# Kernel optimization log

Hardware: AMD Instinct MI355X
Metric: run time of the kernel (lower is better)

The kernel has to match this reference:

```python
import jax, jax.numpy as jnp
import numpy as np

N = 10000      # nodes of this type
T = 160000     # total metapath instances (ragged rows)
D = 256        # input_dim
P = 256        # pre_embed_dim
H = 512        # mlp_settings['layer_list'][0]
S = 64         # select_dim


def setup_inputs() -> dict:
    key = jax.random.key(0)
    ks = jax.random.split(key, 16)
    def w(k, shape):
        return jax.random.normal(k, shape, jnp.float32) / np.sqrt(shape[0]).astype(np.float32)
    return {
        "feat_A": jax.random.normal(ks[0], (N, D), jnp.float32),
        "feat_AP": jax.random.normal(ks[1], (T, D), jnp.float32),
        "feat_APA": jax.random.normal(ks[2], (T, 2 * D), jnp.float32),
        "seg_AP": jnp.sort(jax.random.randint(ks[3], (T,), 0, N, jnp.int32)),
        "seg_APA": jnp.sort(jax.random.randint(ks[4], (T,), 0, N, jnp.int32)),
        "type_weight": w(ks[5], (D, P)),
        "W_enc_AP": w(ks[6], (D, H)),   "b_enc_AP": jnp.zeros((H,), jnp.float32),
        "W_dec_AP": w(ks[7], (H, P)),   "b_dec_AP": jnp.zeros((P,), jnp.float32),
        "W_enc_APA": w(ks[8], (2 * D, H)), "b_enc_APA": jnp.zeros((H,), jnp.float32),
        "W_dec_APA": w(ks[9], (H, P)),  "b_dec_APA": jnp.zeros((P,), jnp.float32),
        "W_attn1": w(ks[10], (2 * P, 2 * P)),
        "W_attn2": w(ks[11], (2 * P, 1)),
        "W_cls": w(ks[12], (P, S)), "b_cls": jnp.zeros((S,), jnp.float32),
    }


def reference(feat_A, feat_AP, feat_APA, seg_AP, seg_APA, type_weight,
              W_enc_AP, b_enc_AP, W_dec_AP, b_dec_AP,
              W_enc_APA, b_enc_APA, W_dec_APA, b_dec_APA,
              W_attn1, W_attn2, W_cls, b_cls):
    # center node embedding (metapath of length 1): feat @ type_weight
    center = feat_A @ type_weight                                  # [N, P]

    def metapath_path(feat, seg, We, be, Wd, bd):
        # per-metapath MLP encode (Linear+ReLU) / decode (Linear)
        h = jax.nn.relu(feat @ We + be)                            # [T, H]
        dec = h @ Wd + bd                                          # [T, P]
        # ragged split + per-node sum aggregation; empty segments -> zeros
        return jax.ops.segment_sum(dec, seg, num_segments=N,
                                   indices_are_sorted=True)        # [N, P]

    inj_AP = metapath_path(feat_AP, seg_AP, W_enc_AP, b_enc_AP, W_dec_AP, b_dec_AP)
    inj_APA = metapath_path(feat_APA, seg_APA, W_enc_APA, b_enc_APA, W_dec_APA, b_dec_APA)

    def attn_score(inj):
        # attn = Tanh -> Linear(2P,2P,no bias) -> Linear(2P,1,no bias) -> LeakyReLU(0.1), then mean
        x = jnp.tanh(jnp.concatenate([center, inj], axis=1))       # [N, 2P]
        s = (x @ W_attn1) @ W_attn2                                # [N, 1]
        return jax.nn.leaky_relu(s, 0.1).mean()

    # index 0 corresponds to the length-1 metapath (never scored; fixed to 0)
    scores = jnp.stack([jnp.zeros((), jnp.float32), attn_score(inj_AP), attn_score(inj_APA)])
    wts = jax.nn.softmax(scores)                                   # [3]

    inj_AP = inj_AP * wts[1]
    inj_APA = inj_APA * wts[2]
    embed = (inj_AP + inj_APA) * 0.5                               # stack(...,dim=2).mean(dim=2)
    pre_embed = jax.nn.log_softmax((center + embed) @ W_cls + b_cls, axis=1)  # [N, S]
    return pre_embed, inj_AP, inj_APA
```

## Files before the change

### kernel.cpp

```cpp
#include <hip/hip_runtime.h>
#include <stdint.h>

typedef __bf16 bf16x8 __attribute__((ext_vector_type(8)));
typedef __bf16 bf16x4 __attribute__((ext_vector_type(4)));
typedef float  f32x4  __attribute__((ext_vector_type(4)));

#define N_NODES 10000
#define T_ROWS  160000
#define HDIM    512
#define PDIM    256
#define NCTILES 157

__device__ __forceinline__ f32x4 mfma16(bf16x8 a, bf16x8 b, f32x4 c) {
    return __builtin_amdgcn_mfma_f32_16x16x32_bf16(a, b, c, 0, 0, 0);
}

__device__ __forceinline__ void pack_one(const float* __restrict__ W,
                                         __bf16* __restrict__ out,
                                         int K, int Nc, int ltid) {
    int lane = ltid & 63;
    int t = ltid >> 6;
    int KT = K >> 5;
    int kt = t % KT, nt = t / KT;
    int col = (nt << 4) + (lane & 15);
    int krow = (kt << 5) + ((lane >> 4) << 3);
    __bf16* dst = out + ((size_t)ltid << 3);
#pragma unroll
    for (int e = 0; e < 8; ++e)
        dst[e] = (__bf16)W[(size_t)(krow + e) * Nc + col];
}

__global__ void pack6_kernel(
    const float* __restrict__ tw,    __bf16* __restrict__ twP,
    const float* __restrict__ WeAP,  __bf16* __restrict__ WeAPp,
    const float* __restrict__ WdAP,  __bf16* __restrict__ WdAPp,
    const float* __restrict__ WeAPA, __bf16* __restrict__ WeAPAp,
    const float* __restrict__ WdAPA, __bf16* __restrict__ WdAPAp,
    const float* __restrict__ W1, const float* __restrict__ W2,
    float* __restrict__ vbuf)
{
    int tid = blockIdx.x * 512 + threadIdx.x;
    if      (tid <  8192) pack_one(tw,    twP,    256, 256, tid);
    else if (tid < 24576) pack_one(WeAP,  WeAPp,  256, 512, tid - 8192);
    else if (tid < 40960) pack_one(WdAP,  WdAPp,  512, 256, tid - 24576);
    else if (tid < 73728) pack_one(WeAPA, WeAPAp, 512, 512, tid - 40960);
    else if (tid < 90112) pack_one(WdAPA, WdAPAp, 512, 256, tid - 73728);
    else if (tid < 90624) {
        int k = tid - 90112;
        float s = 0.f;
        for (int j = 0; j < 512; ++j) s += W1[k * 512 + j] * W2[j];
        vbuf[k] = s;
    }
}

template<int DIN>
__device__ __forceinline__ void path_body(
    const float* __restrict__ X,
    const __bf16* __restrict__ WeP, const float* __restrict__ be,
    const __bf16* __restrict__ WdP, const float* __restrict__ bd,
    const int* __restrict__ seg,
    float* __restrict__ inj,
    int tile, __bf16* buf, int* segs)
{
    constexpr int LDX = DIN + 8;
    constexpr int LDH = HDIM + 8;
    constexpr int LDP = 260;
    constexpr int KT1 = DIN / 32;
    const int tid = threadIdx.x;
    const int row0 = tile * 64;
    if (tid < 64) segs[tid] = seg[row0 + tid];

#pragma unroll 4
    for (int i = tid; i < 64 * (DIN / 4); i += 512) {
        int r = i / (DIN / 4), c4 = i % (DIN / 4);
        float4 f = ((const float4*)X)[(size_t)(row0 + r) * (DIN / 4) + c4];
        bf16x4 h;
        h[0] = (__bf16)f.x; h[1] = (__bf16)f.y; h[2] = (__bf16)f.z; h[3] = (__bf16)f.w;
        *(bf16x4*)&buf[r * LDX + c4 * 4] = h;
    }
    __syncthreads();

    const int wave = tid >> 6, lane = tid & 63;
    const int lr = lane & 15, lg = lane >> 4;

    f32x4 acc1[4][4] = {};
    {
        const __bf16* w1 = WeP + ((size_t)(wave * 4) * KT1) * 512 + lane * 8;
        bf16x8 bX[4], bY[4], a[4];
#pragma unroll
        for (int ct = 0; ct < 4; ++ct) bX[ct] = *(const bf16x8*)&w1[(size_t)(ct * KT1) * 512];
        for (int kt = 0; kt < KT1; kt += 2) {
#pragma unroll
            for (int ct = 0; ct < 4; ++ct)
                bY[ct] = *(const bf16x8*)&w1[(size_t)(ct * KT1 + kt + 1) * 512];
            int ko = kt * 32 + lg * 8;
#pragma unroll
            for (int rt = 0; rt < 4; ++rt)
                a[rt] = *(const bf16x8*)&buf[(rt * 16 + lr) * LDX + ko];
            __builtin_amdgcn_s_setprio(1);
#pragma unroll
            for (int ct = 0; ct < 4; ++ct)
#pragma unroll
                for (int rt = 0; rt < 4; ++rt)
                    acc1[rt][ct] = mfma16(a[rt], bX[ct], acc1[rt][ct]);
            __builtin_amdgcn_s_setprio(0);
            int kn = (kt + 2 < KT1) ? kt + 2 : 0;
#pragma unroll
            for (int ct = 0; ct < 4; ++ct)
                bX[ct] = *(const bf16x8*)&w1[(size_t)(ct * KT1 + kn) * 512];
            ko = (kt + 1) * 32 + lg * 8;
#pragma unroll
            for (int rt = 0; rt < 4; ++rt)
                a[rt] = *(const bf16x8*)&buf[(rt * 16 + lr) * LDX + ko];
            __builtin_amdgcn_s_setprio(1);
#pragma unroll
            for (int ct = 0; ct < 4; ++ct)
#pragma unroll
                for (int rt = 0; rt < 4; ++rt)
                    acc1[rt][ct] = mfma16(a[rt], bY[ct], acc1[rt][ct]);
            __builtin_amdgcn_s_setprio(0);
        }
    }
    __syncthreads();

#pragma unroll
    for (int ct = 0; ct < 4; ++ct) {
        int col = wave * 64 + ct * 16 + lr;
        float bias = be[col];
#pragma unroll
        for (int rt = 0; rt < 4; ++rt) {
            int rbase = rt * 16 + lg * 4;
#pragma unroll
            for (int j = 0; j < 4; ++j) {
                float vl = acc1[rt][ct][j] + bias;
                buf[(rbase + j) * LDH + col] = (__bf16)(vl > 0.f ? vl : 0.f);
            }
        }
    }
    __syncthreads();

    f32x4 acc2[4][2] = {};
    {
        const __bf16* w2 = WdP + ((size_t)(wave * 2) * 16) * 512 + lane * 8;
        bf16x8 bX2[2], bY2[2], aX[4], aY[4];
#pragma unroll
        for (int ct = 0; ct < 2; ++ct) bX2[ct] = *(const bf16x8*)&w2[(size_t)(ct * 16) * 512];
#pragma unroll
        for (int rt = 0; rt < 4; ++rt)
            aX[rt] = *(const bf16x8*)&buf[(rt * 16 + lr) * LDH + lg * 8];
        for (int kt = 0; kt < 16; kt += 2) {
#pragma unroll
            for (int ct = 0; ct < 2; ++ct)
                bY2[ct] = *(const bf16x8*)&w2[(size_t)(ct * 16 + kt + 1) * 512];
            int ko = (kt + 1) * 32 + lg * 8;
#pragma unroll
            for (int rt = 0; rt < 4; ++rt)
                aY[rt] = *(const bf16x8*)&buf[(rt * 16 + lr) * LDH + ko];
            __builtin_amdgcn_s_setprio(1);
#pragma unroll
            for (int ct = 0; ct < 2; ++ct)
#pragma unroll
                for (int rt = 0; rt < 4; ++rt)
                    acc2[rt][ct] = mfma16(aX[rt], bX2[ct], acc2[rt][ct]);
            __builtin_amdgcn_s_setprio(0);
            int kn = (kt + 2 < 16) ? kt + 2 : 0;
#pragma unroll
            for (int ct = 0; ct < 2; ++ct)
                bX2[ct] = *(const bf16x8*)&w2[(size_t)(ct * 16 + kn) * 512];
            ko = kn * 32 + lg * 8;
#pragma unroll
            for (int rt = 0; rt < 4; ++rt)
                aX[rt] = *(const bf16x8*)&buf[(rt * 16 + lr) * LDH + ko];
            __builtin_amdgcn_s_setprio(1);
#pragma unroll
            for (int ct = 0; ct < 2; ++ct)
#pragma unroll
                for (int rt = 0; rt < 4; ++rt)
                    acc2[rt][ct] = mfma16(aY[rt], bY2[ct], acc2[rt][ct]);
            __builtin_amdgcn_s_setprio(0);
        }
    }
    __syncthreads();

    float* decs = (float*)buf;
#pragma unroll
    for (int ct = 0; ct < 2; ++ct) {
        int col = wave * 32 + ct * 16 + lr;
        float bias = bd[col];
#pragma unroll
        for (int rt = 0; rt < 4; ++rt) {
            int rbase = rt * 16 + lg * 4;
#pragma unroll
            for (int j = 0; j < 4; ++j)
                decs[(rbase + j) * LDP + col] = acc2[rt][ct][j] + bias;
        }
    }

    {
        const int c  = wave * 32 + (lane & 31);
        const int rs = (lane >> 5) * 32;
        float run = decs[rs * LDP + c];
        int cur = segs[rs];
        int runstart = rs;
#pragma unroll
        for (int r = rs + 1; r < rs + 32; ++r) {
            int s = segs[r];
            float v = decs[r * LDP + c];
            if (s == cur) run += v;
            else {
                if (runstart != rs) inj[(size_t)cur * PDIM + c] = run;
                else atomicAdd(&inj[(size_t)cur * PDIM + c], run);
                cur = s; run = v; runstart = r;
            }
        }
        atomicAdd(&inj[(size_t)cur * PDIM + c], run);
    }
}

__device__ __forceinline__ void center_body(
    const float* __restrict__ feat, const __bf16* __restrict__ twP,
    float* __restrict__ center, int tile, __bf16* xs)
{
    constexpr int LDX = 264;
    const int tid = threadIdx.x;
    const int row0 = tile * 64;
#pragma unroll 4
    for (int i = tid; i < 64 * 64; i += 512) {
        int r = i / 64, c4 = i % 64;
        int row = row0 + r;
        float4 f = {0.f, 0.f, 0.f, 0.f};
        if (row < N_NODES) f = ((const float4*)feat)[(size_t)row * 64 + c4];
        bf16x4 h;
        h[0] = (__bf16)f.x; h[1] = (__bf16)f.y; h[2] = (__bf16)f.z; h[3] = (__bf16)f.w;
        *(bf16x4*)&xs[r * LDX + c4 * 4] = h;
    }
    __syncthreads();

    const int wave = tid >> 6, lane = tid & 63;
    const int lr = lane & 15, lg = lane >> 4;
    f32x4 acc[4][2] = {};
    const __bf16* w = twP + ((size_t)(wave * 2) * 8) * 512 + lane * 8;
    for (int kt = 0; kt < 8; ++kt) {
        int ko = kt * 32 + lg * 8;
        bf16x8 a[4];
#pragma unroll
        for (int rt = 0; rt < 4; ++rt)
            a[rt] = *(const bf16x8*)&xs[(rt * 16 + lr) * LDX + ko];
#pragma unroll
        for (int ct = 0; ct < 2; ++ct) {
            bf16x8 b = *(const bf16x8*)&w[(size_t)(ct * 8 + kt) * 512];
#pragma unroll
            for (int rt = 0; rt < 4; ++rt)
                acc[rt][ct] = mfma16(a[rt], b, acc[rt][ct]);
        }
    }
#pragma unroll
    for (int ct = 0; ct < 2; ++ct) {
        int col = wave * 32 + ct * 16 + lr;
#pragma unroll
        for (int rt = 0; rt < 4; ++rt) {
            int rbase = rt * 16 + lg * 4;
#pragma unroll
            for (int j = 0; j < 4; ++j) {
                int row = row0 + rbase + j;
                if (row < N_NODES) center[(size_t)row * 256 + col] = acc[rt][ct][j];
            }
        }
    }
}

__global__ __launch_bounds__(512, 4) void paths_kernel(
    const float* __restrict__ featAP,  const float* __restrict__ featAPA,
    const __bf16* __restrict__ WeAPp,  const float* __restrict__ beAP,
    const __bf16* __restrict__ WdAPp,  const float* __restrict__ bdAP,
    const __bf16* __restrict__ WeAPAp, const float* __restrict__ beAPA,
    const __bf16* __restrict__ WdAPAp, const float* __restrict__ bdAPA,
    const int* __restrict__ segAP, const int* __restrict__ segAPA,
    float* __restrict__ injAP, float* __restrict__ injAPA,
    const float* __restrict__ featA, const __bf16* __restrict__ twP,
    float* __restrict__ center)
{
    __shared__ __bf16 buf[64 * (HDIM + 8)];
    __shared__ int segs[64];
    int bid = blockIdx.x;
    if (bid < NCTILES) {
        center_body(featA, twP, center, bid, buf);
        return;
    }
    int p = bid - NCTILES;
    int tile = p >> 1;
    if (p & 1)
        path_body<512>(featAPA, WeAPAp, beAPA, WdAPAp, bdAPA, segAPA, injAPA,
                       tile, buf, segs);
    else
        path_body<256>(featAP, WeAPp, beAP, WdAPp, bdAP, segAP, injAP,
                       tile, buf, segs);
}

__global__ __launch_bounds__(256, 4) void score2_kernel(
    const float* __restrict__ center, const float* __restrict__ injAP,
    const float* __restrict__ injAPA, const float* __restrict__ v,
    float* __restrict__ sacc)
{
    const int w = threadIdx.x >> 6, lane = threadIdx.x & 63;
    float l1 = 0.f, l2 = 0.f;
    for (int row = blockIdx.x * 4 + w; row < N_NODES; row += gridDim.x * 4) {
        float x1 = 0.f, x2 = 0.f;
#pragma unroll
        for (int k = 0; k < 4; ++k) {
            int c = lane + k * 64;
            size_t off = (size_t)row * 256 + c;
            float tc = tanhf(center[off]) * v[c];
            float vi = v[256 + c];
            x1 += tc + tanhf(injAP[off]) * vi;
            x2 += tc + tanhf(injAPA[off]) * vi;
        }
#pragma unroll
        for (int o = 32; o > 0; o >>= 1) {
            x1 += __shfl_xor(x1, o);
            x2 += __shfl_xor(x2, o);
        }
        if (lane == 0) {
            l1 += (x1 > 0.f) ? x1 : 0.1f * x1;
            l2 += (x2 > 0.f) ? x2 : 0.1f * x2;
        }
    }
    if (lane == 0) {
        atomicAdd(&sacc[0], l1);
        atomicAdd(&sacc[1], l2);
    }
}

__global__ __launch_bounds__(256, 4) void final_kernel(
    const float* __restrict__ center, const float* __restrict__ injAP,
    const float* __restrict__ injAPA, const float* __restrict__ sacc,
    const float* __restrict__ Wcls, const float* __restrict__ bcls,
    float* __restrict__ out0, float* __restrict__ out1, float* __restrict__ out2)
{
    __shared__ float zs[4][256];
    float s1 = sacc[0] * (1.f / N_NODES), s2 = sacc[1] * (1.f / N_NODES);
    float m0 = fmaxf(0.f, fmaxf(s1, s2));
    float e0 = expf(0.f - m0), e1 = expf(s1 - m0), e2 = expf(s2 - m0);
    float inv = 1.f / (e0 + e1 + e2);
    const float w1 = e1 * inv, w2 = e2 * inv;

    const int row0 = blockIdx.x * 4;
    for (int idx = threadIdx.x; idx < 1024; idx += 256) {
        int r = idx >> 8, c = idx & 255;
        size_t off = (size_t)(row0 + r) * 256 + c;
        float a = injAP[off] * w1, b = injAPA[off] * w2;
        out1[off] = a; out2[off] = b;
        zs[r][c] = center[off] + 0.5f * (a + b);
    }
    __syncthreads();
    const int g = threadIdx.x >> 6, j = threadIdx.x & 63;
    float logit = bcls[j];
    for (int k = 0; k < 256; ++k) logit += zs[g][k] * Wcls[k * 64 + j];
    float m = logit;
#pragma unroll
    for (int o = 32; o > 0; o >>= 1) m = fmaxf(m, __shfl_xor(m, o));
    float e = expf(logit - m);
    float se = e;
#pragma unroll
    for (int o = 32; o > 0; o >>= 1) se += __shfl_xor(se, o);
    out0[(size_t)(row0 + g) * 64 + j] = (logit - m) - logf(se);
}

extern "C" void kernel_launch(void* const* d_in, const int* in_sizes, int n_in,
                              void* d_out, int out_size, void* d_ws, size_t ws_size,
                              hipStream_t stream)
{
    const float* feat_A   = (const float*)d_in[0];
    const float* feat_AP  = (const float*)d_in[1];
    const float* feat_APA = (const float*)d_in[2];
    const int*   seg_AP   = (const int*)d_in[3];
    const int*   seg_APA  = (const int*)d_in[4];
    const float* type_w   = (const float*)d_in[5];
    const float* We_AP    = (const float*)d_in[6];
    const float* be_AP    = (const float*)d_in[7];
    const float* Wd_AP    = (const float*)d_in[8];
    const float* bd_AP    = (const float*)d_in[9];
    const float* We_APA   = (const float*)d_in[10];
    const float* be_APA   = (const float*)d_in[11];
    const float* Wd_APA   = (const float*)d_in[12];
    const float* bd_APA   = (const float*)d_in[13];
    const float* W_attn1  = (const float*)d_in[14];
    const float* W_attn2  = (const float*)d_in[15];
    const float* W_cls    = (const float*)d_in[16];
    const float* b_cls    = (const float*)d_in[17];

    char* ws = (char*)d_ws;
    size_t o = 0;
    auto alloc = [&](size_t bytes) { char* p = ws + o; o += (bytes + 255) & ~size_t(255); return p; };
    float* center = (float*)alloc((size_t)N_NODES * 256 * 4);
    float* injAP  = (float*)alloc((size_t)N_NODES * 256 * 4);
    float* injAPA = (float*)alloc((size_t)N_NODES * 256 * 4);
    float* vbuf   = (float*)alloc(512 * 4);
    float* sacc   = (float*)alloc(256);
    __bf16* twP    = (__bf16*)alloc(256 * 256 * 2);
    __bf16* WeAPp  = (__bf16*)alloc(256 * 512 * 2);
    __bf16* WdAPp  = (__bf16*)alloc(512 * 256 * 2);
    __bf16* WeAPAp = (__bf16*)alloc(512 * 512 * 2);
    __bf16* WdAPAp = (__bf16*)alloc(512 * 256 * 2);

    hipMemsetAsync(injAP,  0, (size_t)N_NODES * 256 * 4, stream);
    hipMemsetAsync(injAPA, 0, (size_t)N_NODES * 256 * 4, stream);
    hipMemsetAsync(sacc,   0, 256, stream);

    pack6_kernel<<<177, 512, 0, stream>>>(type_w, twP, We_AP, WeAPp, Wd_AP, WdAPp,
                                          We_APA, WeAPAp, Wd_APA, WdAPAp,
                                          W_attn1, W_attn2, vbuf);
    paths_kernel<<<NCTILES + 2 * (T_ROWS / 64), 512, 0, stream>>>(
        feat_AP, feat_APA, WeAPp, be_AP, WdAPp, bd_AP,
        WeAPAp, be_APA, WdAPAp, bd_APA, seg_AP, seg_APA, injAP, injAPA,
        feat_A, twP, center);
    score2_kernel<<<256, 256, 0, stream>>>(center, injAP, injAPA, vbuf, sacc);

    float* out0 = (float*)d_out;
    float* out1 = out0 + (size_t)N_NODES * 64;
    float* out2 = out1 + (size_t)N_NODES * 256;
    final_kernel<<<N_NODES / 4, 256, 0, stream>>>(center, injAP, injAPA, sacc,
                                                  W_cls, b_cls, out0, out1, out2);
}
```

Measured before the change: 426.6 us.

## Make path kernel persistent with register-prefetched next tile and split LDS buffers

Replaces one-block-per-tile launch with 256 persistent blocks, statically partitioned between the AP and APA paths, each looping over tiles with a stride. The next tile's features and segment ids are loaded into registers during the first GEMM and written to a separate x buffer, overlapping global loads with MFMA work. The center-embedding tiles are folded into the AP blocks after their path work. This doubles LDS use, drops launch bounds occupancy to 2, raises register pressure from the prefetch, and fixes the AP/APA block ratio by hand.

After: 1.165 ms. +173.0%, slower.

```diff
diff --git a/kernel.cpp b/kernel.cpp
--- a/kernel.cpp
+++ b/kernel.cpp
@@ -9,7 +9,10 @@
 #define T_ROWS  160000
 #define HDIM    512
 #define PDIM    256
+#define NTILES  2500
 #define NCTILES 157
+#define NBLK_AP  102
+#define NBLK_APA 154
 
 __device__ __forceinline__ f32x4 mfma16(bf16x8 a, bf16x8 b, f32x4 c) {
     return __builtin_amdgcn_mfma_f32_16x16x32_bf16(a, b, c, 0, 0, 0);
@@ -54,166 +57,196 @@
 }
 
 template<int DIN>
-__device__ __forceinline__ void path_body(
+__device__ __forceinline__ void path_persist(
     const float* __restrict__ X,
     const __bf16* __restrict__ WeP, const float* __restrict__ be,
     const __bf16* __restrict__ WdP, const float* __restrict__ bd,
     const int* __restrict__ seg,
     float* __restrict__ inj,
-    int tile, __bf16* buf, int* segs)
+    int t0, int stride,
+    __bf16* xbuf, __bf16* hbuf, int* segsA, int* segsB)
 {
     constexpr int LDX = DIN + 8;
     constexpr int LDH = HDIM + 8;
     constexpr int LDP = 260;
     constexpr int KT1 = DIN / 32;
+    constexpr int NB  = DIN / 32;
     const int tid = threadIdx.x;
-    const int row0 = tile * 64;
-    if (tid < 64) segs[tid] = seg[row0 + tid];
-
-#pragma unroll 4
-    for (int i = tid; i < 64 * (DIN / 4); i += 512) {
-        int r = i / (DIN / 4), c4 = i % (DIN / 4);
-        float4 f = ((const float4*)X)[(size_t)(row0 + r) * (DIN / 4) + c4];
-        bf16x4 h;
-        h[0] = (__bf16)f.x; h[1] = (__bf16)f.y; h[2] = (__bf16)f.z; h[3] = (__bf16)f.w;
-        *(bf16x4*)&buf[r * LDX + c4 * 4] = h;
-    }
-    __syncthreads();
-
     const int wave = tid >> 6, lane = tid & 63;
     const int lr = lane & 15, lg = lane >> 4;
 
-    f32x4 acc1[4][4] = {};
     {
-        const __bf16* w1 = WeP + ((size_t)(wave * 4) * KT1) * 512 + lane * 8;
-        bf16x8 bX[4], bY[4], a[4];
-#pragma unroll
-        for (int ct = 0; ct < 4; ++ct) bX[ct] = *(const bf16x8*)&w1[(size_t)(ct * KT1) * 512];
-        for (int kt = 0; kt < KT1; kt += 2) {
-#pragma unroll
-            for (int ct = 0; ct < 4; ++ct)
-                bY[ct] = *(const bf16x8*)&w1[(size_t)(ct * KT1 + kt + 1) * 512];
-            int ko = kt * 32 + lg * 8;
+        const float4* Xv = (const float4*)X + (size_t)t0 * 64 * (DIN / 4);
+#pragma unroll
+        for (int k = 0; k < NB; ++k) {
+            int i = tid + k * 512, r = i / (DIN / 4), c4 = i % (DIN / 4);
+            float4 f = Xv[i];
+            bf16x4 h;
+            h[0] = (__bf16)f.x; h[1] = (__bf16)f.y; h[2] = (__bf16)f.z; h[3] = (__bf16)f.w;
+            *(bf16x4*)&xbuf[r * LDX + c4 * 4] = h;
+        }
+        if (tid < 64) segsA[tid] = seg[t0 * 64 + tid];
+    }
+    __syncthreads();
+
+    int parity = 0;
+    for (int t = t0; t < NTILES; t += stride, parity ^= 1) {
+        const int tn = t + stride;
+        const bool hasNext = tn < NTILES;
+        int* segsCur = parity ? segsB : segsA;
+        int* segsNxt = parity ? segsA : segsB;
+
+        float4 xh[NB];
+        int segv = 0;
+        if (hasNext) {
+            const float4* Xv = (const float4*)X + (size_t)tn * 64 * (DIN / 4);
+#pragma unroll
+            for (int k = 0; k < NB; ++k) xh[k] = Xv[tid + k * 512];
+            if (tid < 64) segv = seg[tn * 64 + tid];
+        }
+
+        f32x4 acc1[4][4] = {};
+        {
+            const __bf16* w1 = WeP + ((size_t)(wave * 4) * KT1) * 512 + lane * 8;
+            bf16x8 bX[4], bY[4], a[4];
+#pragma unroll
+            for (int ct = 0; ct < 4; ++ct) bX[ct] = *(const bf16x8*)&w1[(size_t)(ct * KT1) * 512];
+            for (int kt = 0; kt < KT1; kt += 2) {
+#pragma unroll
+                for (int ct = 0; ct < 4; ++ct)
+                    bY[ct] = *(const bf16x8*)&w1[(size_t)(ct * KT1 + kt + 1) * 512];
+                int ko = kt * 32 + lg * 8;
+#pragma unroll
+                for (int rt = 0; rt < 4; ++rt)
+                    a[rt] = *(const bf16x8*)&xbuf[(rt * 16 + lr) * LDX + ko];
+                __builtin_amdgcn_s_setprio(1);
+#pragma unroll
+                for (int ct = 0; ct < 4; ++ct)
+#pragma unroll
+                    for (int rt = 0; rt < 4; ++rt)
+                        acc1[rt][ct] = mfma16(a[rt], bX[ct], acc1[rt][ct]);
+                __builtin_amdgcn_s_setprio(0);
+                int kn = (kt + 2 < KT1) ? kt + 2 : 0;
+#pragma unroll
+                for (int ct = 0; ct < 4; ++ct)
+                    bX[ct] = *(const bf16x8*)&w1[(size_t)(ct * KT1 + kn) * 512];
+                ko = (kt + 1) * 32 + lg * 8;
+#pragma unroll
+                for (int rt = 0; rt < 4; ++rt)
+                    a[rt] = *(const bf16x8*)&xbuf[(rt * 16 + lr) * LDX + ko];
+                __builtin_amdgcn_s_setprio(1);
+#pragma unroll
+                for (int ct = 0; ct < 4; ++ct)
+#pragma unroll
+                    for (int rt = 0; rt < 4; ++rt)
+                        acc1[rt][ct] = mfma16(a[rt], bY[ct], acc1[rt][ct]);
+                __builtin_amdgcn_s_setprio(0);
+            }
+        }
+        __syncthreads();
+
+        if (hasNext) {
+#pragma unroll
+            for (int k = 0; k < NB; ++k) {
+                int i = tid + k * 512, r = i / (DIN / 4), c4 = i % (DIN / 4);
+                bf16x4 h;
+                h[0] = (__bf16)xh[k].x; h[1] = (__bf16)xh[k].y;
+                h[2] = (__bf16)xh[k].z; h[3] = (__bf16)xh[k].w;
+                *(bf16x4*)&xbuf[r * LDX + c4 * 4] = h;
+            }
+            if (tid < 64) segsNxt[tid] = segv;
+        }
+#pragma unroll
+        for (int ct = 0; ct < 4; ++ct) {
+            int col = wave * 64 + ct * 16 + lr;
+            float bias = be[col];
+#pragma unroll
+            for (int rt = 0; rt < 4; ++rt) {
+                int rbase = rt * 16 + lg * 4;
+#pragma unroll
+                for (int j = 0; j < 4; ++j) {
+                    float vl = acc1[rt][ct][j] + bias;
+                    hbuf[(rbase + j) * LDH + col] = (__bf16)(vl > 0.f ? vl : 0.f);
+                }
+            }
+        }
+        __syncthreads();
+
+        f32x4 acc2[4][2] = {};
+        {
+            const __bf16* w2 = WdP + ((size_t)(wave * 2) * 16) * 512 + lane * 8;
+            bf16x8 bX2[2], bY2[2], aX[4], aY[4];
+#pragma unroll
+            for (int ct = 0; ct < 2; ++ct) bX2[ct] = *(const bf16x8*)&w2[(size_t)(ct * 16) * 512];
 #pragma unroll
             for (int rt = 0; rt < 4; ++rt)
-                a[rt] = *(const bf16x8*)&buf[(rt * 16 + lr) * LDX + ko];
-            __builtin_amdgcn_s_setprio(1);
-#pragma unroll
-            for (int ct = 0; ct < 4; ++ct)
+                aX[rt] = *(const bf16x8*)&hbuf[(rt * 16 + lr) * LDH + lg * 8];
+            for (int kt = 0; kt < 16; kt += 2) {
+#pragma unroll
+                for (int ct = 0; ct < 2; ++ct)
+                    bY2[ct] = *(const bf16x8*)&w2[(size_t)(ct * 16 + kt + 1) * 512];
+                int ko = (kt + 1) * 32 + lg * 8;
 #pragma unroll
                 for (int rt = 0; rt < 4; ++rt)
-                    acc1[rt][ct] = mfma16(a[rt], bX[ct], acc1[rt][ct]);
-            __builtin_amdgcn_s_setprio(0);
-            int kn = (kt + 2 < KT1) ? kt + 2 : 0;
-#pragma unroll
-            for (int ct = 0; ct < 4; ++ct)
-                bX[ct] = *(const bf16x8*)&w1[(size_t)(ct * KT1 + kn) * 512];
-            ko = (kt + 1) * 32 + lg * 8;
-#pragma unroll
-            for (int rt = 0; rt < 4; ++rt)
-                a[rt] = *(const bf16x8*)&buf[(rt * 16 + lr) * LDX + ko];
-            __builtin_amdgcn_s_setprio(1);
-#pragma unroll
-            for (int ct = 0; ct < 4; ++ct)
+                    aY[rt] = *(const bf16x8*)&hbuf[(rt * 16 + lr) * LDH + ko];
+                __builtin_amdgcn_s_setprio(1);
+#pragma unroll
+                for (int ct = 0; ct < 2; ++ct)
+#pragma unroll
+                    for (int rt = 0; rt < 4; ++rt)
+                        acc2[rt][ct] = mfma16(aX[rt], bX2[ct], acc2[rt][ct]);
+                __builtin_amdgcn_s_setprio(0);
+                int kn = (kt + 2 < 16) ? kt + 2 : 0;
+#pragma unroll
+                for (int ct = 0; ct < 2; ++ct)
+                    bX2[ct] = *(const bf16x8*)&w2[(size_t)(ct * 16 + kn) * 512];
+                ko = kn * 32 + lg * 8;
 #pragma unroll
                 for (int rt = 0; rt < 4; ++rt)
-                    acc1[rt][ct] = mfma16(a[rt], bY[ct], acc1[rt][ct]);
-            __builtin_amdgcn_s_setprio(0);
-        }
-    }
-    __syncthreads();
-
-#pragma unroll
-    for (int ct = 0; ct < 4; ++ct) {
-        int col = wave * 64 + ct * 16 + lr;
-        float bias = be[col];
-#pragma unroll
-        for (int rt = 0; rt < 4; ++rt) {
-            int rbase = rt * 16 + lg * 4;
-#pragma unroll
-            for (int j = 0; j < 4; ++j) {
-                float vl = acc1[rt][ct][j] + bias;
-                buf[(rbase + j) * LDH + col] = (__bf16)(vl > 0.f ? vl : 0.f);
-            }
-        }
-    }
-    __syncthreads();
-
-    f32x4 acc2[4][2] = {};
-    {
-        const __bf16* w2 = WdP + ((size_t)(wave * 2) * 16) * 512 + lane * 8;
-        bf16x8 bX2[2], bY2[2], aX[4], aY[4];
-#pragma unroll
-        for (int ct = 0; ct < 2; ++ct) bX2[ct] = *(const bf16x8*)&w2[(size_t)(ct * 16) * 512];
-#pragma unroll
-        for (int rt = 0; rt < 4; ++rt)
-            aX[rt] = *(const bf16x8*)&buf[(rt * 16 + lr) * LDH + lg * 8];
-        for (int kt = 0; kt < 16; kt += 2) {
-#pragma unroll
-            for (int ct = 0; ct < 2; ++ct)
-                bY2[ct] = *(const bf16x8*)&w2[(size_t)(ct * 16 + kt + 1) * 512];
-            int ko = (kt + 1) * 32 + lg * 8;
-#pragma unroll
-            for (int rt = 0; rt < 4; ++rt)
-                aY[rt] = *(const bf16x8*)&buf[(rt * 16 + lr) * LDH + ko];
-            __builtin_amdgcn_s_setprio(1);
-#pragma unroll
-            for (int ct = 0; ct < 2; ++ct)
-#pragma unroll
-                for (int rt = 0; rt < 4; ++rt)
-                    acc2[rt][ct] = mfma16(aX[rt], bX2[ct], acc2[rt][ct]);
-            __builtin_amdgcn_s_setprio(0);
-            int kn = (kt + 2 < 16) ? kt + 2 : 0;
-#pragma unroll
-            for (int ct = 0; ct < 2; ++ct)
-                bX2[ct] = *(const bf16x8*)&w2[(size_t)(ct * 16 + kn) * 512];
-            ko = kn * 32 + lg * 8;
-#pragma unroll
-            for (int rt = 0; rt < 4; ++rt)
-                aX[rt] = *(const bf16x8*)&buf[(rt * 16 + lr) * LDH + ko];
-            __builtin_amdgcn_s_setprio(1);
-#pragma unroll
-            for (int ct = 0; ct < 2; ++ct)
-#pragma unroll
-                for (int rt = 0; rt < 4; ++rt)
-                    acc2[rt][ct] = mfma16(aY[rt], bY2[ct], acc2[rt][ct]);
-            __builtin_amdgcn_s_setprio(0);
-        }
-    }
-    __syncthreads();
-
-    float* decs = (float*)buf;
-#pragma unroll
-    for (int ct = 0; ct < 2; ++ct) {
-        int col = wave * 32 + ct * 16 + lr;
-        float bias = bd[col];
-#pragma unroll
-        for (int rt = 0; rt < 4; ++rt) {
-            int rbase = rt * 16 + lg * 4;
-#pragma unroll
-            for (int j = 0; j < 4; ++j)
-                decs[(rbase + j) * LDP + col] = acc2[rt][ct][j] + bias;
-        }
-    }
-
-    {
-        const int c  = wave * 32 + (lane & 31);
-        const int rs = (lane >> 5) * 32;
-        float run = decs[rs * LDP + c];
-        int cur = segs[rs];
-        int runstart = rs;
-#pragma unroll
-        for (int r = rs + 1; r < rs + 32; ++r) {
-            int s = segs[r];
-            float v = decs[r * LDP + c];
-            if (s == cur) run += v;
-            else {
-                if (runstart != rs) inj[(size_t)cur * PDIM + c] = run;
-                else atomicAdd(&inj[(size_t)cur * PDIM + c], run);
-                cur = s; run = v; runstart = r;
-            }
-        }
-        atomicAdd(&inj[(size_t)cur * PDIM + c], run);
+                    aX[rt] = *(const bf16x8*)&hbuf[(rt * 16 + lr) * LDH + ko];
+                __builtin_amdgcn_s_setprio(1);
+#pragma unroll
+                for (int ct = 0; ct < 2; ++ct)
+#pragma unroll
+                    for (int rt = 0; rt < 4; ++rt)
+                        acc2[rt][ct] = mfma16(aY[rt], bY2[ct], acc2[rt][ct]);
+                __builtin_amdgcn_s_setprio(0);
+            }
+        }
+        __syncthreads();
+
+        float* decs = (float*)hbuf;
+#pragma unroll
+        for (int ct = 0; ct < 2; ++ct) {
+            int col = wave * 32 + ct * 16 + lr;
+            float bias = bd[col];
+#pragma unroll
+            for (int rt = 0; rt < 4; ++rt) {
+                int rbase = rt * 16 + lg * 4;
+#pragma unroll
+                for (int j = 0; j < 4; ++j)
+                    decs[(rbase + j) * LDP + col] = acc2[rt][ct][j] + bias;
+            }
+        }
+        {
+            const int c  = wave * 32 + (lane & 31);
+            const int rs = (lane >> 5) * 32;
+            float run = decs[rs * LDP + c];
+            int cur = segsCur[rs];
+            int runstart = rs;
+#pragma unroll
+            for (int r = rs + 1; r < rs + 32; ++r) {
+                int s = segsCur[r];
+                float v = decs[r * LDP + c];
+                if (s == cur) run += v;
+                else {
+                    if (runstart != rs) inj[(size_t)cur * PDIM + c] = run;
+                    else atomicAdd(&inj[(size_t)cur * PDIM + c], run);
+                    cur = s; run = v; runstart = r;
+                }
+            }
+            atomicAdd(&inj[(size_t)cur * PDIM + c], run);
+        }
     }
 }
 
@@ -224,6 +257,7 @@
     constexpr int LDX = 264;
     const int tid = threadIdx.x;
     const int row0 = tile * 64;
+    __syncthreads();
 #pragma unroll 4
     for (int i = tid; i < 64 * 64; i += 512) {
         int r = i / 64, c4 = i % 64;
@@ -269,7 +303,7 @@
     }
 }
 
-__global__ __launch_bounds__(512, 4) void paths_kernel(
+__global__ __launch_bounds__(512, 2) void paths_kernel(
     const float* __restrict__ featAP,  const float* __restrict__ featAPA,
     const __bf16* __restrict__ WeAPp,  const float* __restrict__ beAP,
     const __bf16* __restrict__ WdAPp,  const float* __restrict__ bdAP,
@@ -280,21 +314,19 @@
     const float* __restrict__ featA, const __bf16* __restrict__ twP,
     float* __restrict__ center)
 {
-    __shared__ __bf16 buf[64 * (HDIM + 8)];
-    __shared__ int segs[64];
-    int bid = blockIdx.x;
-    if (bid < NCTILES) {
-        center_body(featA, twP, center, bid, buf);
-        return;
-    }
-    int p = bid - NCTILES;
-    int tile = p >> 1;
-    if (p & 1)
-        path_body<512>(featAPA, WeAPAp, beAPA, WdAPAp, bdAPA, segAPA, injAPA,
-                       tile, buf, segs);
-    else
-        path_body<256>(featAP, WeAPp, beAP, WdAPp, bdAP, segAP, injAP,
-                       tile, buf, segs);
+    __shared__ __bf16 xbuf[64 * (HDIM + 8)];
+    __shared__ __bf16 hbuf[64 * (HDIM + 8)];
+    __shared__ int segsA[64], segsB[64];
+    int b = blockIdx.x;
+    if (b < NBLK_AP) {
+        path_persist<256>(featAP, WeAPp, beAP, WdAPp, bdAP, segAP, injAP,
+                          b, NBLK_AP, xbuf, hbuf, segsA, segsB);
+        for (int c = b; c < NCTILES; c += NBLK_AP)
+            center_body(featA, twP, center, c, xbuf);
+    } else {
+        path_persist<512>(featAPA, WeAPAp, beAPA, WdAPAp, bdAPA, segAPA, injAPA,
+                          b - NBLK_AP, NBLK_APA, xbuf, hbuf, segsA, segsB);
+    }
 }
 
 __global__ __launch_bounds__(256, 4) void score2_kernel(
@@ -410,7 +442,7 @@
     pack6_kernel<<<177, 512, 0, stream>>>(type_w, twP, We_AP, WeAPp, Wd_AP, WdAPp,
                                           We_APA, WeAPAp, Wd_APA, WdAPAp,
                                           W_attn1, W_attn2, vbuf);
-    paths_kernel<<<NCTILES + 2 * (T_ROWS / 64), 512, 0, stream>>>(
+    paths_kernel<<<NBLK_AP + NBLK_APA, 512, 0, stream>>>(
         feat_AP, feat_APA, WeAPp, be_AP, WdAPp, bd_AP,
         WeAPAp, be_APA, WdAPAp, bd_APA, seg_AP, seg_APA, injAP, injAPA,
         feat_A, twP, center);
```

## Double path-kernel row tile to 128 rows per block for weight reuse

Applied to the files above, without the earlier changes.

Each path block now processes 128 metapath rows instead of 64, so every weight fragment loaded from global memory feeds twice as many MFMAs. The input load is batched into 8 outstanding float4 loads before conversion, and center tiles are moved to the end of the grid. LDS use per block doubles (about 133KB) and accumulators double, so launch bounds drop to 2 blocks per CU, which reduces occupancy and latency hiding. The segmented reduction now scans 64 rows per thread.

Result: slower. 446.3 us (+4.6%).

```diff
diff --git a/kernel.cpp b/kernel.cpp
--- a/kernel.cpp
+++ b/kernel.cpp
@@ -9,6 +9,8 @@
 #define T_ROWS  160000
 #define HDIM    512
 #define PDIM    256
+#define BM      128
+#define NPT     1250
 #define NCTILES 157
 
 __device__ __forceinline__ f32x4 mfma16(bf16x8 a, bf16x8 b, f32x4 c) {
@@ -66,27 +68,44 @@
     constexpr int LDH = HDIM + 8;
     constexpr int LDP = 260;
     constexpr int KT1 = DIN / 32;
+    constexpr int NB4 = BM * (DIN / 4) / 512;
     const int tid = threadIdx.x;
-    const int row0 = tile * 64;
-    if (tid < 64) segs[tid] = seg[row0 + tid];
-
-#pragma unroll 4
-    for (int i = tid; i < 64 * (DIN / 4); i += 512) {
-        int r = i / (DIN / 4), c4 = i % (DIN / 4);
-        float4 f = ((const float4*)X)[(size_t)(row0 + r) * (DIN / 4) + c4];
-        bf16x4 h;
-        h[0] = (__bf16)f.x; h[1] = (__bf16)f.y; h[2] = (__bf16)f.z; h[3] = (__bf16)f.w;
-        *(bf16x4*)&buf[r * LDX + c4 * 4] = h;
+    const int row0 = tile * BM;
+    if (tid < BM) segs[tid] = seg[row0 + tid];
+
+    {
+        const float4* Xv = (const float4*)X + (size_t)row0 * (DIN / 4);
+#pragma unroll
+        for (int bb = 0; bb < NB4 / 8; ++bb) {
+            float4 tmp[8];
+#pragma unroll
+            for (int k = 0; k < 8; ++k)
+                tmp[k] = Xv[tid + (bb * 8 + k) * 512];
+#pragma unroll
+            for (int k = 0; k < 8; ++k) {
+                int i = tid + (bb * 8 + k) * 512;
+                int r = i / (DIN / 4), c4 = i % (DIN / 4);
+                bf16x4 h;
+                h[0] = (__bf16)tmp[k].x; h[1] = (__bf16)tmp[k].y;
+                h[2] = (__bf16)tmp[k].z; h[3] = (__bf16)tmp[k].w;
+                *(bf16x4*)&buf[r * LDX + c4 * 4] = h;
+            }
+        }
     }
     __syncthreads();
 
     const int wave = tid >> 6, lane = tid & 63;
     const int lr = lane & 15, lg = lane >> 4;
 
-    f32x4 acc1[4][4] = {};
+    f32x4 acc[8][4];
+#pragma unroll
+    for (int rt = 0; rt < 8; ++rt)
+#pragma unroll
+        for (int ct = 0; ct < 4; ++ct) acc[rt][ct] = (f32x4){0.f, 0.f, 0.f, 0.f};
+
     {
         const __bf16* w1 = WeP + ((size_t)(wave * 4) * KT1) * 512 + lane * 8;
-        bf16x8 bX[4], bY[4], a[4];
+        bf16x8 bX[4], bY[4], a[8];
 #pragma unroll
         for (int ct = 0; ct < 4; ++ct) bX[ct] = *(const bf16x8*)&w1[(size_t)(ct * KT1) * 512];
         for (int kt = 0; kt < KT1; kt += 2) {
@@ -95,14 +114,14 @@
                 bY[ct] = *(const bf16x8*)&w1[(size_t)(ct * KT1 + kt + 1) * 512];
             int ko = kt * 32 + lg * 8;
 #pragma unroll
-            for (int rt = 0; rt < 4; ++rt)
+            for (int rt = 0; rt < 8; ++rt)
                 a[rt] = *(const bf16x8*)&buf[(rt * 16 + lr) * LDX + ko];
             __builtin_amdgcn_s_setprio(1);
 #pragma unroll
             for (int ct = 0; ct < 4; ++ct)
 #pragma unroll
-                for (int rt = 0; rt < 4; ++rt)
-                    acc1[rt][ct] = mfma16(a[rt], bX[ct], acc1[rt][ct]);
+                for (int rt = 0; rt < 8; ++rt)
+                    acc[rt][ct] = mfma16(a[rt], bX[ct], acc[rt][ct]);
             __builtin_amdgcn_s_setprio(0);
             int kn = (kt + 2 < KT1) ? kt + 2 : 0;
 #pragma unroll
@@ -110,14 +129,14 @@
                 bX[ct] = *(const bf16x8*)&w1[(size_t)(ct * KT1 + kn) * 512];
             ko = (kt + 1) * 32 + lg * 8;
 #pragma unroll
-            for (int rt = 0; rt < 4; ++rt)
+            for (int rt = 0; rt < 8; ++rt)
                 a[rt] = *(const bf16x8*)&buf[(rt * 16 + lr) * LDX + ko];
             __builtin_amdgcn_s_setprio(1);
 #pragma unroll
             for (int ct = 0; ct < 4; ++ct)
 #pragma unroll
-                for (int rt = 0; rt < 4; ++rt)
-                    acc1[rt][ct] = mfma16(a[rt], bY[ct], acc1[rt][ct]);
+                for (int rt = 0; rt < 8; ++rt)
+                    acc[rt][ct] = mfma16(a[rt], bY[ct], acc[rt][ct]);
             __builtin_amdgcn_s_setprio(0);
         }
     }
@@ -128,55 +147,55 @@
         int col = wave * 64 + ct * 16 + lr;
         float bias = be[col];
 #pragma unroll
-        for (int rt = 0; rt < 4; ++rt) {
+        for (int rt = 0; rt < 8; ++rt) {
             int rbase = rt * 16 + lg * 4;
 #pragma unroll
             for (int j = 0; j < 4; ++j) {
-                float vl = acc1[rt][ct][j] + bias;
+                float vl = acc[rt][ct][j] + bias;
                 buf[(rbase + j) * LDH + col] = (__bf16)(vl > 0.f ? vl : 0.f);
             }
         }
     }
     __syncthreads();
 
-    f32x4 acc2[4][2] = {};
+#pragma unroll
+    for (int rt = 0; rt < 8; ++rt)
+#pragma unroll
+        for (int ct = 0; ct < 2; ++ct) acc[rt][ct] = (f32x4){0.f, 0.f, 0.f, 0.f};
     {
         const __bf16* w2 = WdP + ((size_t)(wave * 2) * 16) * 512 + lane * 8;
-        bf16x8 bX2[2], bY2[2], aX[4], aY[4];
+        bf16x8 bX2[2], bY2[2], a[8];
 #pragma unroll
         for (int ct = 0; ct < 2; ++ct) bX2[ct] = *(const bf16x8*)&w2[(size_t)(ct * 16) * 512];
-#pragma unroll
-        for (int rt = 0; rt < 4; ++rt)
-            aX[rt] = *(const bf16x8*)&buf[(rt * 16 + lr) * LDH + lg * 8];
         for (int kt = 0; kt < 16; kt += 2) {
 #pragma unroll
             for (int ct = 0; ct < 2; ++ct)
                 bY2[ct] = *(const bf16x8*)&w2[(size_t)(ct * 16 + kt + 1) * 512];
-            int ko = (kt + 1) * 32 + lg * 8;
-#pragma unroll
-            for (int rt = 0; rt < 4; ++rt)
-                aY[rt] = *(const bf16x8*)&buf[(rt * 16 + lr) * LDH + ko];
+            int ko = kt * 32 + lg * 8;
+#pragma unroll
+            for (int rt = 0; rt < 8; ++rt)
+                a[rt] = *(const bf16x8*)&buf[(rt * 16 + lr) * LDH + ko];
             __builtin_amdgcn_s_setprio(1);
 #pragma unroll
             for (int ct = 0; ct < 2; ++ct)
 #pragma unroll
-                for (int rt = 0; rt < 4; ++rt)
-                    acc2[rt][ct] = mfma16(aX[rt], bX2[ct], acc2[rt][ct]);
+                for (int rt = 0; rt < 8; ++rt)
+                    acc[rt][ct] = mfma16(a[rt], bX2[ct], acc[rt][ct]);
             __builtin_amdgcn_s_setprio(0);
             int kn = (kt + 2 < 16) ? kt + 2 : 0;
 #pragma unroll
             for (int ct = 0; ct < 2; ++ct)
                 bX2[ct] = *(const bf16x8*)&w2[(size_t)(ct * 16 + kn) * 512];
-            ko = kn * 32 + lg * 8;
-#pragma unroll
-            for (int rt = 0; rt < 4; ++rt)
-                aX[rt] = *(const bf16x8*)&buf[(rt * 16 + lr) * LDH + ko];
+            ko = (kt + 1) * 32 + lg * 8;
+#pragma unroll
+            for (int rt = 0; rt < 8; ++rt)
+                a[rt] = *(const bf16x8*)&buf[(rt * 16 + lr) * LDH + ko];
             __builtin_amdgcn_s_setprio(1);
 #pragma unroll
             for (int ct = 0; ct < 2; ++ct)
 #pragma unroll
-                for (int rt = 0; rt < 4; ++rt)
-                    acc2[rt][ct] = mfma16(aY[rt], bY2[ct], acc2[rt][ct]);
+                for (int rt = 0; rt < 8; ++rt)
+                    acc[rt][ct] = mfma16(a[rt], bY2[ct], acc[rt][ct]);
             __builtin_amdgcn_s_setprio(0);
         }
     }
@@ -188,22 +207,22 @@
         int col = wave * 32 + ct * 16 + lr;
         float bias = bd[col];
 #pragma unroll
-        for (int rt = 0; rt < 4; ++rt) {
+        for (int rt = 0; rt < 8; ++rt) {
             int rbase = rt * 16 + lg * 4;
 #pragma unroll
             for (int j = 0; j < 4; ++j)
-                decs[(rbase + j) * LDP + col] = acc2[rt][ct][j] + bias;
+                decs[(rbase + j) * LDP + col] = acc[rt][ct][j] + bias;
         }
     }
 
     {
         const int c  = wave * 32 + (lane & 31);
-        const int rs = (lane >> 5) * 32;
+        const int rs = (lane >> 5) * 64;
         float run = decs[rs * LDP + c];
         int cur = segs[rs];
         int runstart = rs;
-#pragma unroll
-        for (int r = rs + 1; r < rs + 32; ++r) {
+#pragma unroll 8
+        for (int r = rs + 1; r < rs + 64; ++r) {
             int s = segs[r];
             float v = decs[r * LDP + c];
             if (s == cur) run += v;
@@ -269,7 +288,7 @@
     }
 }
 
-__global__ __launch_bounds__(512, 4) void paths_kernel(
+__global__ __launch_bounds__(512, 2) void paths_kernel(
     const float* __restrict__ featAP,  const float* __restrict__ featAPA,
     const __bf16* __restrict__ WeAPp,  const float* __restrict__ beAP,
     const __bf16* __restrict__ WdAPp,  const float* __restrict__ bdAP,
@@ -280,16 +299,15 @@
     const float* __restrict__ featA, const __bf16* __restrict__ twP,
     float* __restrict__ center)
 {
-    __shared__ __bf16 buf[64 * (HDIM + 8)];
-    __shared__ int segs[64];
+    __shared__ __bf16 buf[BM * (HDIM + 8)];
+    __shared__ int segs[BM];
     int bid = blockIdx.x;
-    if (bid < NCTILES) {
-        center_body(featA, twP, center, bid, buf);
+    if (bid >= 2 * NPT) {
+        center_body(featA, twP, center, bid - 2 * NPT, buf);
         return;
     }
-    int p = bid - NCTILES;
-    int tile = p >> 1;
-    if (p & 1)
+    int tile = bid >> 1;
+    if (bid & 1)
         path_body<512>(featAPA, WeAPAp, beAPA, WdAPAp, bdAPA, segAPA, injAPA,
                        tile, buf, segs);
     else
@@ -410,7 +428,7 @@
     pack6_kernel<<<177, 512, 0, stream>>>(type_w, twP, We_AP, WeAPp, Wd_AP, WdAPp,
                                           We_APA, WeAPAp, Wd_APA, WdAPAp,
                                           W_attn1, W_attn2, vbuf);
-    paths_kernel<<<NCTILES + 2 * (T_ROWS / 64), 512, 0, stream>>>(
+    paths_kernel<<<2 * NPT + NCTILES, 512, 0, stream>>>(
         feat_AP, feat_APA, WeAPp, be_AP, WdAPp, bd_AP,
         WeAPAp, be_APA, WdAPAp, bd_APA, seg_AP, seg_APA, injAP, injAPA,
         feat_A, twP, center);
```
